# Kernel optimization log

Hardware: AMD Instinct MI355X
Metric: run time of the kernel (lower is better)

Reference implementation:

```python
import jax, jax.numpy as jnp
import numpy as np

N = 16384      # nodes (256 chess boards x 64 squares)
E = 393216     # edges (avg degree 24)
G = 256        # graphs
HID = 128
H = 4
C = 32         # head dim
L = 8          # 4 blocks x 2 GATv2Conv
NODE_DIM = 21
EDGE_DIM = 6


def setup_inputs() -> dict:
    key = jax.random.key(0)
    ks = jax.random.split(key, 12)
    x = jax.random.normal(ks[0], (N, NODE_DIM), jnp.float32)
    edge_index = jax.random.randint(ks[1], (2, E), 0, N, dtype=jnp.int32)
    edge_attr = jax.random.uniform(ks[2], (E, EDGE_DIM), dtype=jnp.float32)
    batch = jnp.sort(jax.random.randint(ks[3], (N,), 0, G, dtype=jnp.int32))

    def w(k, shape, fan_in):
        return jax.random.normal(k, shape, jnp.float32) * (1.0 / np.sqrt(fan_in))

    Win = w(ks[4], (NODE_DIM, HID), NODE_DIM)
    b_in = jnp.zeros((HID,), jnp.float32)
    Wl = w(ks[5], (L, HID, HID), HID)
    bl = jnp.zeros((L, HID), jnp.float32)
    Wr = w(ks[6], (L, HID, HID), HID)
    br = jnp.zeros((L, HID), jnp.float32)
    We = w(ks[7], (L, EDGE_DIM, HID), EDGE_DIM)
    att = w(ks[8], (L, H, C), C)
    bconv = jnp.zeros((L, HID), jnp.float32)
    gamma = jnp.ones((L, HID), jnp.float32)
    beta = jnp.zeros((L, HID), jnp.float32)
    W1 = w(ks[9], (HID, 64), HID)
    b1 = jnp.zeros((64,), jnp.float32)
    W2 = w(ks[10], (64, 3), 64)
    b2 = jnp.zeros((3,), jnp.float32)
    return dict(x=x, edge_index=edge_index, edge_attr=edge_attr, batch=batch,
                Win=Win, b_in=b_in, Wl=Wl, bl=bl, Wr=Wr, br=br, We=We, att=att,
                bconv=bconv, gamma=gamma, beta=beta, W1=W1, b1=b1, W2=W2, b2=b2)


def _gatv2(h, src, dst, ea, Wl, bl, Wr, br, We, att, bias):
    # PyG GATv2Conv: message j->i uses x_j from lin_l, x_i from lin_r
    xl = (h @ Wl + bl).reshape(N, H, C)
    xr = (h @ Wr + br).reshape(N, H, C)
    ee = (ea @ We).reshape(-1, H, C)
    m = jax.nn.leaky_relu(xl[src] + xr[dst] + ee, 0.2)   # [Ef, H, C]
    s = jnp.einsum('ehc,hc->eh', m, att)                 # [Ef, H]
    smax = jax.ops.segment_max(s, dst, num_segments=N)   # self-loops => no empty segs
    ex = jnp.exp(s - smax[dst])
    den = jax.ops.segment_sum(ex, dst, num_segments=N)
    alpha = ex / den[dst]                                # edge softmax per target node
    out = jax.ops.segment_sum(alpha[:, :, None] * xl[src], dst, num_segments=N)
    return out.reshape(N, HID) + bias


def _bn(x, g, b):
    mu = jnp.mean(x, axis=0)
    var = jnp.var(x, axis=0)
    return g * (x - mu) * jax.lax.rsqrt(var + 1e-5) + b


def reference(x, edge_index, edge_attr, batch, Win, b_in, Wl, bl, Wr, br, We, att,
              bconv, gamma, beta, W1, b1, W2, b2):
    src0, dst0 = edge_index[0], edge_index[1]
    # add self-loops with fill_value='mean' (per-target mean of incoming edge_attr)
    deg = jax.ops.segment_sum(jnp.ones((E,), jnp.float32), dst0, num_segments=N)
    loop_attr = jax.ops.segment_sum(edge_attr, dst0, num_segments=N) / jnp.maximum(deg, 1.0)[:, None]
    idx = jnp.arange(N, dtype=src0.dtype)
    src = jnp.concatenate([src0, idx])
    dst = jnp.concatenate([dst0, idx])
    ea = jnp.concatenate([edge_attr, loop_attr], axis=0)

    h = jax.nn.relu(x @ Win + b_in)
    for blk in range(4):
        res = h
        l = 2 * blk
        h = jax.nn.relu(_bn(_gatv2(h, src, dst, ea, Wl[l], bl[l], Wr[l], br[l], We[l], att[l], bconv[l]), gamma[l], beta[l]))
        l = 2 * blk + 1
        h = _bn(_gatv2(h, src, dst, ea, Wl[l], bl[l], Wr[l], br[l], We[l], att[l], bconv[l]), gamma[l], beta[l])
        h = jax.nn.relu(h + res)

    cnt = jnp.maximum(jax.ops.segment_sum(jnp.ones((N,), jnp.float32), batch, num_segments=G), 1.0)
    pooled = jax.ops.segment_sum(h, batch, num_segments=G) / cnt[:, None]
    logits = jax.nn.relu(pooled @ W1 + b1) @ W2 + b2
    return logits
```

## Files before the change

### kernel.cpp

```cpp
#include <hip/hip_runtime.h>
#include <hip/hip_fp16.h>
#include <math.h>

constexpr int N   = 16384;
constexpr int E   = 393216;
constexpr int G   = 256;
constexpr int HID = 128;
constexpr int SLOT = 64;

typedef float fv2 __attribute__((ext_vector_type(2)));

__device__ __forceinline__ float red16(float x) {
    union fi { float f; int i; };
    fi a, b;
    a.f = x;
    b.i = __builtin_amdgcn_mov_dpp(a.i, 0x121, 0xf, 0xf, false); a.f += b.f;
    b.i = __builtin_amdgcn_mov_dpp(a.i, 0x122, 0xf, 0xf, false); a.f += b.f;
    b.i = __builtin_amdgcn_mov_dpp(a.i, 0x124, 0xf, 0xf, false); a.f += b.f;
    b.i = __builtin_amdgcn_mov_dpp(a.i, 0x128, 0xf, 0xf, false); a.f += b.f;
    return a.f;
}

__global__ __launch_bounds__(256) void k_scatter(const int* __restrict__ src,
                                                 const int* __restrict__ dst,
                                                 int* __restrict__ fill,
                                                 const float* __restrict__ edge_attr,
                                                 int* __restrict__ csr_src,
                                                 float* __restrict__ csr_ea) {
    int e = blockIdx.x * 256 + threadIdx.x;
    if (e >= E) return;
    int d = dst[e];
    int pos = atomicAdd(&fill[d], 1);
    if (pos > 62) return;
    size_t base = (size_t)d * SLOT + pos;
    csr_src[base] = src[e];
    const float* s = edge_attr + (size_t)e * 6;
    float4 a = {s[0], s[1], s[2], s[3]};
    float4 b = {s[4], s[5], 0.0f, 0.0f};
    float4* dstp = (float4*)(csr_ea + base * 8);
    dstp[0] = a;
    dstp[1] = b;
}

__global__ __launch_bounds__(256) void k_loopattr2(const int* __restrict__ fill,
                                                   int* __restrict__ csr_src,
                                                   float* __restrict__ csr_ea) {
    int i = blockIdx.x * 256 + threadIdx.x;
    if (i >= N) return;
    int deg = fill[i];
    deg = deg > 62 ? 62 : deg;
    size_t e0 = (size_t)i * SLOT;
    float4 sa = {0, 0, 0, 0};
    float sbx = 0.0f, sby = 0.0f;
    for (int e = 0; e < deg; e++) {
        const float4* p = (const float4*)(csr_ea + (e0 + e) * 8);
        float4 a = p[0];
        float4 b = p[1];
        sa.x += a.x; sa.y += a.y; sa.z += a.z; sa.w += a.w;
        sbx += b.x; sby += b.y;
    }
    float inv = 1.0f / fmaxf((float)deg, 1.0f);
    float4 oa = {sa.x * inv, sa.y * inv, sa.z * inv, sa.w * inv};
    float4 ob = {sbx * inv, sby * inv, 0.0f, 0.0f};
    float4* q = (float4*)(csr_ea + (e0 + deg) * 8);
    q[0] = oa;
    q[1] = ob;
    csr_src[e0 + deg] = i;
}

__global__ __launch_bounds__(128) void k_ingemm(const float* __restrict__ x,
                                                const float* __restrict__ Win,
                                                const float* __restrict__ b_in,
                                                float* __restrict__ h) {
    __shared__ float xs[21];
    int i = blockIdx.x;
    int c = threadIdx.x;
    if (c < 21) xs[c] = x[i * 21 + c];
    __syncthreads();
    float acc = b_in[c];
#pragma unroll
    for (int d = 0; d < 21; d++) acc += xs[d] * Win[d * HID + c];
    h[i * HID + c] = fmaxf(acc, 0.0f);
}

__global__ __launch_bounds__(256) void k_gemm_lr(const float* __restrict__ h,
                                                 const float* __restrict__ bns,
                                                 const float* __restrict__ gamma,
                                                 const float* __restrict__ beta,
                                                 float* __restrict__ res,
                                                 const float* __restrict__ Wl,
                                                 const float* __restrict__ bl,
                                                 const float* __restrict__ Wr,
                                                 const float* __restrict__ br,
                                                 __half2* __restrict__ XLh,
                                                 float* __restrict__ XR) {
    __shared__ float hs[16][HID];
    __shared__ float sc[HID], sh[HID];
    int t = threadIdx.x;
    int r0 = blockIdx.x * 16;
    if (bns) {
        if (t < 128) {
            const float invN = 1.0f / (float)N;
            float mean = bns[t] * invN;
            float var  = bns[128 + t] * invN - mean * mean;
            float inv  = rsqrtf(var + 1e-5f);
            float s = gamma[t] * inv;
            sc[t] = s;
            sh[t] = beta[t] - mean * s;
        }
        __syncthreads();
    }
    {
        int row = t >> 4;
        int col = (t & 15) * 8;
        size_t base = (size_t)(r0 + row) * HID + col;
        const float4* src = (const float4*)&h[base];
        float4 a = src[0];
        float4 b = src[1];
        if (bns) {
            float4 s0 = *(const float4*)&sc[col];
            float4 s1 = *(const float4*)&sc[col + 4];
            float4 h0 = *(const float4*)&sh[col];
            float4 h1 = *(const float4*)&sh[col + 4];
            a.x = fmaf(a.x, s0.x, h0.x);
            a.y = fmaf(a.y, s0.y, h0.y);
            a.z = fmaf(a.z, s0.z, h0.z);
            a.w = fmaf(a.w, s0.w, h0.w);
            b.x = fmaf(b.x, s1.x, h1.x);
            b.y = fmaf(b.y, s1.y, h1.y);
            b.z = fmaf(b.z, s1.z, h1.z);
            b.w = fmaf(b.w, s1.w, h1.w);
            if (res) {
                const float4* rp = (const float4*)&res[base];
                float4 ra = rp[0];
                float4 rb = rp[1];
                a.x += ra.x; a.y += ra.y; a.z += ra.z; a.w += ra.w;
                b.x += rb.x; b.y += rb.y; b.z += rb.z; b.w += rb.w;
            }
            a.x = fmaxf(a.x, 0.0f); a.y = fmaxf(a.y, 0.0f);
            a.z = fmaxf(a.z, 0.0f); a.w = fmaxf(a.w, 0.0f);
            b.x = fmaxf(b.x, 0.0f); b.y = fmaxf(b.y, 0.0f);
            b.z = fmaxf(b.z, 0.0f); b.w = fmaxf(b.w, 0.0f);
            if (res) {
                float4* wp = (float4*)&res[base];
                wp[0] = a;
                wp[1] = b;
            }
        }
        float4* dst = (float4*)&hs[row][col];
        dst[0] = a;
        dst[1] = b;
    }
    __syncthreads();
    bool right = t >= 128;
    int cp = (t & 63) * 2;
    int rbase = ((t >> 6) & 1) * 8;
    const float* W    = right ? Wr : Wl;
    const float* bias = right ? br : bl;
    float b0 = bias[cp], b1 = bias[cp + 1];
    float acc0[8], acc1[8];
#pragma unroll
    for (int r = 0; r < 8; r++) { acc0[r] = b0; acc1[r] = b1; }
    for (int k = 0; k < HID; k += 4) {
        float4 h4[8];
#pragma unroll
        for (int r = 0; r < 8; r++) h4[r] = *(const float4*)&hs[rbase + r][k];
#pragma unroll
        for (int kk = 0; kk < 4; kk++) {
            float2 w = *(const float2*)&W[(size_t)(k + kk) * HID + cp];
#pragma unroll
            for (int r = 0; r < 8; r++) {
                float hv = ((const float*)&h4[r])[kk];
                acc0[r] = fmaf(hv, w.x, acc0[r]);
                acc1[r] = fmaf(hv, w.y, acc1[r]);
            }
        }
    }
    if (right) {
#pragma unroll
        for (int r = 0; r < 8; r++) {
            float2 o = {acc0[r], acc1[r]};
            *(float2*)&XR[(size_t)(r0 + rbase + r) * HID + cp] = o;
        }
    } else {
#pragma unroll
        for (int r = 0; r < 8; r++) {
            XLh[(size_t)(r0 + rbase + r) * 64 + (cp >> 1)] =
                __floats2half2_rn(acc0[r], acc1[r]);
        }
    }
}

__global__ __launch_bounds__(256, 4) void k_edge(const int* __restrict__ fill,
                                                 const int* __restrict__ csr_src,
                                                 const float* __restrict__ csr_ea,
                                                 const __half2* __restrict__ xlh,
                                                 const float* __restrict__ xr,
                                                 const float* __restrict__ We_l,
                                                 const float* __restrict__ att_l,
                                                 float* __restrict__ gout) {
    int i = (blockIdx.x * 256 + threadIdx.x) >> 6;
    int lane = threadIdx.x & 63;
    int hh = lane >> 4;
    int ss = lane & 15;
    int ch0 = hh * 32 + 2 * ss;

    const float LOG2E = 1.44269504088896f;
    float a0 = att_l[ch0] * LOG2E, a1 = att_l[ch0 + 1] * LOG2E;
    fv2 wep[6];
#pragma unroll
    for (int d = 0; d < 6; d++) {
        float2 wv = *(const float2*)&We_l[d * HID + ch0];
        wep[d] = (fv2){wv.x, wv.y};
    }
    float2 xr2 = *(const float2*)&xr[(size_t)i * HID + ch0];
    fv2 xrp = (fv2){xr2.x, xr2.y};

    float rd = 0.0f, acc0 = 0.0f, acc1 = 0.0f;
    int e0 = i * SLOT;
    int deg = __builtin_amdgcn_readfirstlane(fill[i]);
    deg = deg > 62 ? 62 : deg;
    int e1 = e0 + deg + 1;
    int nedge = deg + 1;
    int nfull = nedge >> 2;
    int efull = e0 + (nfull << 2);

    auto ld_idx = [&](int e, int out[4]) {
#pragma unroll
        for (int k = 0; k < 4; k++) {
            int ec = e + k;
            ec = (ec < e1) ? ec : (e1 - 1);
            out[k] = __builtin_amdgcn_readfirstlane(csr_src[ec]);
        }
    };
    auto ld_xl = [&](const int idx[4], __half2 out[4]) {
#pragma unroll
        for (int k = 0; k < 4; k++)
            out[k] = xlh[(size_t)idx[k] * 64 + lane];
    };
    auto ld_ea = [&](int e, float4 outA[4], float2 outB[4]) {
#pragma unroll
        for (int k = 0; k < 4; k++) {
            const float* p = csr_ea + (size_t)(e + k) * 8;
            outA[k] = *(const float4*)p;
            outB[k] = *(const float2*)(p + 4);
        }
    };
    auto edge1 = [&](const __half2 xlv, const float4 eA, const float2 eB,
                     bool valid) {
        float2 xf = __half22float2(xlv);
        fv2 m = xrp;
        m = eA.x * wep[0] + m;
        m = eA.y * wep[1] + m;
        m = eA.z * wep[2] + m;
        m = eA.w * wep[3] + m;
        m = eB.x * wep[4] + m;
        m = eB.y * wep[5] + m;
        m = m + (fv2){xf.x, xf.y};
        fv2 ml = __builtin_elementwise_max(m, m * 0.2f);
        float pv = fmaf(ml[1], a1, ml[0] * a0);
        pv = red16(pv);
        pv = valid ? pv : -INFINITY;
        float ex = exp2f(pv);
        rd += ex;
        acc0 = fmaf(ex, xf.x, acc0);
        acc1 = fmaf(ex, xf.y, acc1);
    };
    auto bodyF = [&](const __half2 xlv[4], const float4 eA[4], const float2 eB[4]) {
#pragma unroll
        for (int k = 0; k < 4; k++) edge1(xlv[k], eA[k], eB[k], true);
    };

    int iA[4], iB[4];
    __half2 x0[4], x1[4];
    float4 A0[4], A1[4];
    float2 B0[4], B1[4];
    ld_idx(e0, iA);
    ld_idx(e0 + 4, iB);
    ld_xl(iA, x0);
    ld_ea(e0, A0, B0);
    int e = e0, nf = nfull;
    while (nf >= 2) {
        ld_idx(e + 8, iA);
        ld_xl(iB, x1);
        ld_ea(e + 4, A1, B1);
        bodyF(x0, A0, B0);
        ld_idx(e + 12, iB);
        ld_xl(iA, x0);
        ld_ea(e + 8, A0, B0);
        bodyF(x1, A1, B1);
        e += 8; nf -= 2;
    }
    if (nf == 1) {
        bodyF(x0, A0, B0);
    }
    int rem = nedge & 3;
    if (rem) {
        int it[4];
        __half2 xt[4];
        ld_idx(efull, it);
        ld_xl(it, xt);
#pragma unroll
        for (int k = 0; k < 4; k++) {
            int ee = efull + k;
            int ec = (ee < e1) ? ee : (e1 - 1);
            const float* p = csr_ea + (size_t)ec * 8;
            float4 eaA = *(const float4*)p;
            float2 eaB = *(const float2*)(p + 4);
            edge1(xt[k], eaA, eaB, ee < e1);
        }
    }
    float inv = 1.0f / rd;
    float2 o = {acc0 * inv, acc1 * inv};
    *(float2*)&gout[(size_t)i * HID + ch0] = o;
}

__global__ __launch_bounds__(256) void k_bnstats(const float* __restrict__ v,
                                                 float* __restrict__ sums) {
    __shared__ float l_s[256], l_q[256];
    int t = threadIdx.x;
    int c = t & 127;
    int half = t >> 7;
    int r = blockIdx.x * 64 + half;
    float s = 0.0f, q = 0.0f;
    for (int it = 0; it < 32; it++, r += 2) {
        float val = v[(size_t)r * HID + c];
        s += val;
        q = fmaf(val, val, q);
    }
    l_s[t] = s; l_q[t] = q;
    __syncthreads();
    if (t < 128) {
        s = l_s[t] + l_s[t + 128];
        atomicAdd(&sums[c], s);
    } else {
        q = l_q[t] + l_q[t - 128];
        atomicAdd(&sums[128 + c], q);
    }
}

__global__ __launch_bounds__(128) void k_pool(const float* __restrict__ gout,
                                              const float* __restrict__ res,
                                              const float* __restrict__ bns,
                                              const float* __restrict__ gamma,
                                              const float* __restrict__ beta,
                                              const int* __restrict__ batch,
                                              const float* __restrict__ W1,
                                              const float* __restrict__ b1,
                                              const float* __restrict__ W2,
                                              const float* __restrict__ b2,
                                              float* __restrict__ out) {
    __shared__ float pooled[HID];
    __shared__ float hid[64];
    __shared__ int bounds[2];
    int g = blockIdx.x;
    int t = threadIdx.x;
    if (t < 2) {
        int target = g + t;
        int lo = 0, hi = N;
        while (lo < hi) {
            int mid = (lo + hi) >> 1;
            if (batch[mid] < target) lo = mid + 1; else hi = mid;
        }
        bounds[t] = lo;
    }
    const float invN = 1.0f / (float)N;
    float mean = bns[t] * invN;
    float var  = bns[128 + t] * invN - mean * mean;
    float scb  = gamma[t] * rsqrtf(var + 1e-5f);
    float shb  = beta[t] - mean * scb;
    __syncthreads();
    int s = bounds[0], e = bounds[1];
    float acc = 0.0f;
    for (int r = s; r < e; r++) {
        float v = fmaf(gout[(size_t)r * HID + t], scb, shb) + res[(size_t)r * HID + t];
        acc += fmaxf(v, 0.0f);
    }
    float cntf = fmaxf((float)(e - s), 1.0f);
    pooled[t] = acc / cntf;
    __syncthreads();
    if (t < 64) {
        float a = b1[t];
#pragma unroll 4
        for (int c = 0; c < HID; c++) a += pooled[c] * W1[c * 64 + t];
        hid[t] = fmaxf(a, 0.0f);
    }
    __syncthreads();
    if (t < 3) {
        float a = b2[t];
#pragma unroll
        for (int j = 0; j < 64; j++) a += hid[j] * W2[j * 3 + t];
        out[g * 3 + t] = a;
    }
}

extern "C" void kernel_launch(void* const* d_in, const int* in_sizes, int n_in,
                              void* d_out, int out_size, void* d_ws, size_t ws_size,
                              hipStream_t stream) {
    const float* x         = (const float*)d_in[0];
    const int*   edge_index= (const int*)d_in[1];
    const float* edge_attr = (const float*)d_in[2];
    const int*   batch     = (const int*)d_in[3];
    const float* Win       = (const float*)d_in[4];
    const float* b_in      = (const float*)d_in[5];
    const float* Wl        = (const float*)d_in[6];
    const float* bl        = (const float*)d_in[7];
    const float* Wr        = (const float*)d_in[8];
    const float* br        = (const float*)d_in[9];
    const float* We        = (const float*)d_in[10];
    const float* att       = (const float*)d_in[11];
    const float* gamma     = (const float*)d_in[13];
    const float* beta      = (const float*)d_in[14];
    const float* W1        = (const float*)d_in[15];
    const float* b1        = (const float*)d_in[16];
    const float* W2        = (const float*)d_in[17];
    const float* b2        = (const float*)d_in[18];
    float* out = (float*)d_out;

    const int* src0 = edge_index;
    const int* dst0 = edge_index + E;

    char* ws = (char*)d_ws;
    size_t off = 0;
    auto alloc = [&](size_t bytes) -> void* {
        void* p = ws + off;
        off += (bytes + 255) & ~(size_t)255;
        return p;
    };
    int*     fill      = (int*)alloc((size_t)N * sizeof(int));
    float*   bnsums    = (float*)alloc((size_t)8 * 256 * sizeof(float));
    int*     csr_src   = (int*)alloc((size_t)N * SLOT * sizeof(int));
    float*   csr_ea    = (float*)alloc((size_t)N * SLOT * 8 * sizeof(float) + 512);
    float*   H0        = (float*)alloc((size_t)N * HID * sizeof(float));
    __half2* XLh       = (__half2*)alloc((size_t)N * 64 * sizeof(__half2));
    float*   XR        = (float*)alloc((size_t)N * HID * sizeof(float));
    float*   GOUT      = (float*)alloc((size_t)N * HID * sizeof(float));

    size_t zbytes = (size_t)N * sizeof(int) + 8 * 256 * sizeof(float);
    hipMemsetAsync(fill, 0, zbytes, stream);
    k_scatter<<<(E + 255) / 256, 256, 0, stream>>>(src0, dst0, fill,
                                                   edge_attr, csr_src, csr_ea);
    k_loopattr2<<<(N + 255) / 256, 256, 0, stream>>>(fill, csr_src, csr_ea);
    k_ingemm<<<N, 128, 0, stream>>>(x, Win, b_in, H0);

    for (int l = 0; l < 8; l++) {
        bool odd = (l & 1) != 0;
        const float* hin;
        const float* bns_in = nullptr;
        const float* g_in = nullptr;
        const float* b_in2 = nullptr;
        float* res = nullptr;
        if (l == 0) {
            hin = H0;
        } else {
            hin = GOUT;
            bns_in = bnsums + (l - 1) * 256;
            g_in  = gamma + (size_t)(l - 1) * HID;
            b_in2 = beta  + (size_t)(l - 1) * HID;
            if (!odd) res = H0;
        }
        k_gemm_lr<<<N / 16, 256, 0, stream>>>(hin, bns_in, g_in, b_in2, res,
                                              Wl + (size_t)l * HID * HID, bl + l * HID,
                                              Wr + (size_t)l * HID * HID, br + l * HID,
                                              XLh, XR);
        k_edge<<<N / 4, 256, 0, stream>>>(fill, csr_src, csr_ea,
                                          XLh, XR,
                                          We + (size_t)l * 6 * HID,
                                          att + (size_t)l * HID, GOUT);
        k_bnstats<<<256, 256, 0, stream>>>(GOUT, bnsums + l * 256);
    }
    k_pool<<<G, 128, 0, stream>>>(GOUT, H0, bnsums + 7 * 256,
                                  gamma + 7 * HID, beta + 7 * HID,
                                  batch, W1, b1, W2, b2, out);
}
```

Measured before the change: 806.4 us.

## Fuse batch-norm statistics into edge kernel with 1024-thread blocks

```diff
diff --git a/kernel.cpp b/kernel.cpp
--- a/kernel.cpp
+++ b/kernel.cpp
@@ -7,8 +7,6 @@
 constexpr int G   = 256;
 constexpr int HID = 128;
 constexpr int SLOT = 64;
-
-typedef float fv2 __attribute__((ext_vector_type(2)));
 
 __device__ __forceinline__ float red16(float x) {
     union fi { float f; int i; };
@@ -191,31 +189,34 @@
     }
 }
 
-__global__ __launch_bounds__(256, 4) void k_edge(const int* __restrict__ fill,
-                                                 const int* __restrict__ csr_src,
-                                                 const float* __restrict__ csr_ea,
-                                                 const __half2* __restrict__ xlh,
-                                                 const float* __restrict__ xr,
-                                                 const float* __restrict__ We_l,
-                                                 const float* __restrict__ att_l,
-                                                 float* __restrict__ gout) {
-    int i = (blockIdx.x * 256 + threadIdx.x) >> 6;
+__global__ __launch_bounds__(1024) void k_edge(const int* __restrict__ fill,
+                                               const int* __restrict__ csr_src,
+                                               const float* __restrict__ csr_ea,
+                                               const __half2* __restrict__ xlh,
+                                               const float* __restrict__ xr,
+                                               const float* __restrict__ We_l,
+                                               const float* __restrict__ att_l,
+                                               float* __restrict__ gout,
+                                               float* __restrict__ bnsums) {
+    __shared__ float red_lds[16][256];
+    int w = threadIdx.x >> 6;
     int lane = threadIdx.x & 63;
     int hh = lane >> 4;
     int ss = lane & 15;
     int ch0 = hh * 32 + 2 * ss;
+    int i = blockIdx.x * 16 + w;
 
     const float LOG2E = 1.44269504088896f;
     float a0 = att_l[ch0] * LOG2E, a1 = att_l[ch0 + 1] * LOG2E;
-    fv2 wep[6];
+    float we0[6], we1[6];
 #pragma unroll
     for (int d = 0; d < 6; d++) {
         float2 wv = *(const float2*)&We_l[d * HID + ch0];
-        wep[d] = (fv2){wv.x, wv.y};
-    }
+        we0[d] = wv.x;
+        we1[d] = wv.y;
+    }
+
     float2 xr2 = *(const float2*)&xr[(size_t)i * HID + ch0];
-    fv2 xrp = (fv2){xr2.x, xr2.y};
-
     float rd = 0.0f, acc0 = 0.0f, acc1 = 0.0f;
     int e0 = i * SLOT;
     int deg = __builtin_amdgcn_readfirstlane(fill[i]);
@@ -249,16 +250,18 @@
     auto edge1 = [&](const __half2 xlv, const float4 eA, const float2 eB,
                      bool valid) {
         float2 xf = __half22float2(xlv);
-        fv2 m = xrp;
-        m = eA.x * wep[0] + m;
-        m = eA.y * wep[1] + m;
-        m = eA.z * wep[2] + m;
-        m = eA.w * wep[3] + m;
-        m = eB.x * wep[4] + m;
-        m = eB.y * wep[5] + m;
-        m = m + (fv2){xf.x, xf.y};
-        fv2 ml = __builtin_elementwise_max(m, m * 0.2f);
-        float pv = fmaf(ml[1], a1, ml[0] * a0);
+        float u0 = eA.x * we0[0], u1 = eA.x * we1[0];
+        u0 = fmaf(eA.y, we0[1], u0); u1 = fmaf(eA.y, we1[1], u1);
+        u0 = fmaf(eA.z, we0[2], u0); u1 = fmaf(eA.z, we1[2], u1);
+        u0 = fmaf(eA.w, we0[3], u0); u1 = fmaf(eA.w, we1[3], u1);
+        u0 = fmaf(eB.x, we0[4], u0); u1 = fmaf(eB.x, we1[4], u1);
+        u0 = fmaf(eB.y, we0[5], u0); u1 = fmaf(eB.y, we1[5], u1);
+        float m0 = xf.x + xr2.x + u0;
+        float m1 = xf.y + xr2.y + u1;
+        m0 = fmaxf(m0, 0.2f * m0);
+        m1 = fmaxf(m1, 0.2f * m1);
+        float pv = m0 * a0;
+        pv = fmaf(m1, a1, pv);
         pv = red16(pv);
         pv = valid ? pv : -INFINITY;
         float ex = exp2f(pv);
@@ -313,29 +316,18 @@
     float inv = 1.0f / rd;
     float2 o = {acc0 * inv, acc1 * inv};
     *(float2*)&gout[(size_t)i * HID + ch0] = o;
-}
-
-__global__ __launch_bounds__(256) void k_bnstats(const float* __restrict__ v,
-                                                 float* __restrict__ sums) {
-    __shared__ float l_s[256], l_q[256];
+
+    red_lds[w][ch0]           = o.x;
+    red_lds[w][ch0 + 1]       = o.y;
+    red_lds[w][128 + ch0]     = o.x * o.x;
+    red_lds[w][128 + ch0 + 1] = o.y * o.y;
+    __syncthreads();
     int t = threadIdx.x;
-    int c = t & 127;
-    int half = t >> 7;
-    int r = blockIdx.x * 64 + half;
-    float s = 0.0f, q = 0.0f;
-    for (int it = 0; it < 32; it++, r += 2) {
-        float val = v[(size_t)r * HID + c];
-        s += val;
-        q = fmaf(val, val, q);
-    }
-    l_s[t] = s; l_q[t] = q;
-    __syncthreads();
-    if (t < 128) {
-        s = l_s[t] + l_s[t + 128];
-        atomicAdd(&sums[c], s);
-    } else {
-        q = l_q[t] + l_q[t - 128];
-        atomicAdd(&sums[128 + c], q);
+    if (t < 256) {
+        float s = 0.0f;
+#pragma unroll
+        for (int q = 0; q < 16; q++) s += red_lds[q][t];
+        atomicAdd(&bnsums[t], s);
     }
 }
 
@@ -463,11 +455,11 @@
                                               Wl + (size_t)l * HID * HID, bl + l * HID,
                                               Wr + (size_t)l * HID * HID, br + l * HID,
                                               XLh, XR);
-        k_edge<<<N / 4, 256, 0, stream>>>(fill, csr_src, csr_ea,
-                                          XLh, XR,
-                                          We + (size_t)l * 6 * HID,
-                                          att + (size_t)l * HID, GOUT);
-        k_bnstats<<<256, 256, 0, stream>>>(GOUT, bnsums + l * 256);
+        k_edge<<<N / 16, 1024, 0, stream>>>(fill, csr_src, csr_ea,
+                                            XLh, XR,
+                                            We + (size_t)l * 6 * HID,
+                                            att + (size_t)l * HID, GOUT,
+                                            bnsums + l * 256);
     }
     k_pool<<<G, 128, 0, stream>>>(GOUT, H0, bnsums + 7 * 256,
                                   gamma + 7 * HID, beta + 7 * HID,
```

Measured after the change: 838.6 us. 4.0% more time.
